# Performance work log

Measured on AMD Instinct MI355X. Metric: run time of the kernel, lower is better.

## Reference

```python
import jax, jax.numpy as jnp
import numpy as np

N = 16384          # points in the (single-batch) cloud
K = 16             # boundary_k
C = 20             # num semantic classes (ScanNet-style)
IGNORE = -1        # ignore_index
BOUNDARY_W = 1.0   # boundary_loss_weight


def setup_inputs() -> dict:
    key = jax.random.key(0)
    k1, k2, k3 = jax.random.split(key, 3)
    coord = jax.random.normal(k1, (N, 3), jnp.float32)
    seg_logits = jax.random.normal(k2, (N, C), jnp.float32)
    segment = jax.random.randint(k3, (N,), 0, C, dtype=jnp.int32)
    return {"coord": coord, "seg_logits": seg_logits, "segment": segment, "offset": N}


def _knn_idx(coord):
    # brute-force kNN (loop=False): exclude self via +inf diagonal
    d2 = jnp.sum(coord * coord, axis=1)                       # [N]
    dist = d2[:, None] + d2[None, :] - 2.0 * (coord @ coord.T)  # [N, N]
    dist = dist + jnp.where(jnp.eye(dist.shape[0], dtype=bool), jnp.inf, 0.0)
    _, idx = jax.lax.top_k(-dist, K)                          # [N, K] neighbor (src) indices per center (dst)
    return idx


def _masked_ce(logp_tgt, mask):
    # mean cross-entropy over masked points (matches torch reduction='mean' w/ ignore_index)
    cnt = jnp.sum(mask)
    s = jnp.sum(jnp.where(mask, logp_tgt, 0.0))
    return jnp.where(cnt > 0, -s / jnp.maximum(cnt, 1).astype(logp_tgt.dtype), 0.0)


def reference(coord, seg_logits, segment, offset):
    # --- boundary mask: knn_graph -> per-edge label diff -> scatter-max to dst ---
    nbr = _knn_idx(coord)                                     # [N, K] src indices, dst = row index
    nbr_seg = segment[nbr]                                    # gather: [N, K]
    valid_pt = segment != IGNORE                              # [N]
    valid = (nbr_seg != IGNORE) & valid_pt[:, None]           # per-edge valid
    diff = valid & (nbr_seg != segment[:, None])              # per-edge label mismatch
    boundary = jnp.any(diff, axis=1)                          # scatter-max over dst == row-wise any

    # --- main loss: cross-entropy with ignore_index ---
    logp = jax.nn.log_softmax(seg_logits, axis=-1)            # [N, C]
    tgt = jnp.clip(segment, 0, C - 1)
    logp_tgt = jnp.take_along_axis(logp, tgt[:, None], axis=1)[:, 0]  # [N]
    main_loss = _masked_ce(logp_tgt, valid_pt)

    # --- boundary loss: CE restricted to boundary points (0 if none) ---
    bmask = boundary & valid_pt
    boundary_loss = _masked_ce(logp_tgt, bmask)

    loss = main_loss + BOUNDARY_W * boundary_loss
    return loss
```

## Files before the change

### kernel.cpp

```cpp
#include <hip/hip_runtime.h>
#include <hip/hip_bf16.h>
#include <math.h>

#define N_PTS 16384
#define KNN   16
#define NCLS  20
#define BND_W 1.0f

#define THREADS 512
#define WAVES   8
#define FR      4
#define RPW     (16 * FR)
#define RPB     (WAVES * RPW)
#define RBLKS   (N_PTS / RPB)
#define CSPLIT  16
#define CAND_PB (N_PTS / CSPLIT)

typedef short  short8 __attribute__((ext_vector_type(8)));
typedef float  f32x4  __attribute__((ext_vector_type(4)));

__device__ __forceinline__ unsigned short f2bf(float x) {
    union { __hip_bfloat16 h; unsigned short u; } cv;
    cv.h = __float2bfloat16(x);
    return cv.u;
}
__device__ __forceinline__ float bf2f(unsigned short b) {
    union { __hip_bfloat16 h; unsigned short u; } cv;
    cv.u = b;
    return __bfloat162float(cv.h);
}

__global__ __launch_bounds__(256) void k_enc(const float* __restrict__ coord,
                                             const int* __restrict__ seg,
                                             unsigned short* __restrict__ aenc,
                                             unsigned short* __restrict__ benc,
                                             int* __restrict__ cnt,
                                             float* __restrict__ accum,
                                             int* __restrict__ done_rb,
                                             unsigned* __restrict__ done_final) {
    const int i = blockIdx.x * 256 + threadIdx.x;
    float x = coord[3 * i], y = coord[3 * i + 1], z = coord[3 * i + 2];
    int lab = seg[i];
    unsigned short xh = f2bf(x), yh = f2bf(y), zh = f2bf(z);
    unsigned short xl = f2bf(x - bf2f(xh));
    unsigned short yl = f2bf(y - bf2f(yh));
    unsigned short zl = f2bf(z - bf2f(zh));
    float h = 0.5f * fmaf(x, x, fmaf(y, y, z * z));
    unsigned short hh = f2bf(h);
    unsigned short hl = f2bf(h - bf2f(hh));
    const unsigned short one = 0x3F80u, nb = 0xC480u;

    __attribute__((aligned(16))) unsigned short a[32], b[32];
    a[0] = xh; a[1] = xl; a[2] = xh;
    a[3] = yh; a[4] = yl; a[5] = yh;
    a[6] = zh; a[7] = zl; a[8] = zh;
    a[9] = one; a[10] = one;
#pragma unroll
    for (int s = 0; s < NCLS; s++) a[11 + s] = (lab == s) ? nb : 0u;
    a[31] = nb;

    b[0] = xh; b[1] = xh; b[2] = xl;
    b[3] = yh; b[4] = yh; b[5] = yl;
    b[6] = zh; b[7] = zh; b[8] = zl;
    b[9]  = hh ^ 0x8000u;
    b[10] = hl ^ 0x8000u;
#pragma unroll
    for (int s = 0; s < NCLS; s++) b[11 + s] = (lab == s) ? one : 0u;
    b[31] = (lab < 0) ? one : 0u;

    short8* ap = (short8*)(aenc + (size_t)i * 32);
    short8* bp = (short8*)(benc + (size_t)i * 32);
#pragma unroll
    for (int kb = 0; kb < 4; kb++) {
        ap[kb] = ((const short8*)a)[kb];
        bp[kb] = ((const short8*)b)[kb];
    }

    cnt[i] = 0;
    if (i < 4) accum[i] = 0.f;
    if (i == 4) *done_final = 0u;
    if (i >= 8 && i < 8 + RBLKS) done_rb[i - 8] = 0;
}

__device__ __forceinline__ float waveReduceSum(float v) {
#pragma unroll
    for (int off = 32; off > 0; off >>= 1) v += __shfl_down(v, off, 64);
    return v;
}

template<bool PASS1>
__global__ __launch_bounds__(THREADS, 4) void k_pass(
    const unsigned short* __restrict__ aenc,
    const unsigned short* __restrict__ benc,
    const int* __restrict__ seg, const float* __restrict__ logits,
    float* __restrict__ smax_part, int* __restrict__ cnt,
    float* __restrict__ accum, int* __restrict__ done_rb,
    unsigned* __restrict__ done_final, float* __restrict__ out)
{
    __shared__ float thr_lds[RPB];
    __shared__ int s_flag;
    const int tid  = threadIdx.x;
    const int lane = tid & 63, wave = tid >> 6;
    const int l15  = lane & 15, l4 = lane >> 4;
    const int rb   = blockIdx.x * RPB;
    const int split = blockIdx.y;
    const int cb   = split * CAND_PB;

    short8 af[FR];
#pragma unroll
    for (int f = 0; f < FR; f++)
        af[f] = *(const short8*)(aenc + (size_t)(rb + wave * RPW + f * 16 + l15) * 32 + l4 * 8);
    if (!PASS1) {
#pragma unroll
        for (int f = 0; f < FR; f++) {
            union { short8 s; unsigned u[4]; } cv_;
            cv_.s = af[f];
            if (l4 == 1) { cv_.u[1] &= 0x0000FFFFu; cv_.u[2] = 0u; cv_.u[3] = 0u; }
            else if (l4 >= 2) { cv_.u[0] = 0u; cv_.u[1] = 0u; cv_.u[2] = 0u; cv_.u[3] = 0u; }
            af[f] = cv_.s;
        }
    }

    float thr[FR][4];
    if (!PASS1) {
        int row = rb + tid;
        float m = smax_part[row];
#pragma unroll
        for (int s = 1; s < CSPLIT; s++) m = fmaxf(m, smax_part[s * N_PTS + row]);
        thr_lds[tid] = m;
        __syncthreads();
#pragma unroll
        for (int f = 0; f < FR; f++)
#pragma unroll
            for (int r = 0; r < 4; r++)
                thr[f][r] = thr_lds[wave * RPW + f * 16 + l4 * 4 + r];
    }

    f32x4 rmax[FR];
    int cv[FR][4];
#pragma unroll
    for (int f = 0; f < FR; f++)
#pragma unroll
        for (int r = 0; r < 4; r++) { rmax[f][r] = -3.0e38f; cv[f][r] = 0; }

    const short8* bp = (const short8*)benc;
    const f32x4 zero = {0.f, 0.f, 0.f, 0.f};
#pragma unroll 4
    for (int c0 = 0; c0 < CAND_PB; c0 += 16) {
        short8 bf = bp[(size_t)(cb + c0 + l15) * 4 + l4];
        f32x4 d[FR];
#pragma unroll
        for (int f = 0; f < FR; f++)
            d[f] = __builtin_amdgcn_mfma_f32_16x16x32_bf16(af[f], bf, zero, 0, 0, 0);
        if (PASS1) {
#pragma unroll
            for (int f = 0; f < FR; f++)
#pragma unroll
                for (int r = 0; r < 4; r++)
                    rmax[f][r] = fmaxf(rmax[f][r], d[f][r]);
        } else {
#pragma unroll
            for (int f = 0; f < FR; f++)
#pragma unroll
                for (int r = 0; r < 4; r++)
                    cv[f][r] += (d[f][r] > thr[f][r]) ? 1 : 0;
        }
    }

    if (PASS1) {
#pragma unroll
        for (int m = 1; m < 16; m <<= 1)
#pragma unroll
            for (int f = 0; f < FR; f++)
#pragma unroll
                for (int r = 0; r < 4; r++)
                    rmax[f][r] = fmaxf(rmax[f][r], __shfl_xor(rmax[f][r], m, 64));
        if (l15 == 0) {
#pragma unroll
            for (int f = 0; f < FR; f++)
#pragma unroll
                for (int r = 0; r < 4; r++)
                    smax_part[split * N_PTS + rb + wave * RPW + f * 16 + l4 * 4 + r] = rmax[f][r];
        }
    } else {
#pragma unroll
        for (int m = 1; m < 16; m <<= 1)
#pragma unroll
            for (int f = 0; f < FR; f++)
#pragma unroll
                for (int r = 0; r < 4; r++)
                    cv[f][r] += __shfl_xor(cv[f][r], m, 64);
        if (l15 == 0) {
#pragma unroll
            for (int f = 0; f < FR; f++)
#pragma unroll
                for (int r = 0; r < 4; r++)
                    atomicAdd(&cnt[rb + wave * RPW + f * 16 + l4 * 4 + r], cv[f][r]);
        }

        __syncthreads();
        if (tid == 0) {
            __threadfence();
            s_flag = (atomicAdd(&done_rb[blockIdx.x], 1) == CSPLIT - 1) ? 1 : 0;
        }
        __syncthreads();
        if (s_flag) {
            const int row = rb + tid;
            int sg = seg[row];
            bool valid = (sg != -1);
            const float4* row4 = (const float4*)(logits + (size_t)row * NCLS);
            float a[NCLS];
            float4 v0 = row4[0], v1 = row4[1], v2 = row4[2], v3 = row4[3], v4 = row4[4];
            a[0]=v0.x; a[1]=v0.y; a[2]=v0.z; a[3]=v0.w;
            a[4]=v1.x; a[5]=v1.y; a[6]=v1.z; a[7]=v1.w;
            a[8]=v2.x; a[9]=v2.y; a[10]=v2.z; a[11]=v2.w;
            a[12]=v3.x; a[13]=v3.y; a[14]=v3.z; a[15]=v3.w;
            a[16]=v4.x; a[17]=v4.y; a[18]=v4.z; a[19]=v4.w;
            float mx = a[0];
#pragma unroll
            for (int c = 1; c < NCLS; c++) mx = fmaxf(mx, a[c]);
            float se = 0.f;
#pragma unroll
            for (int c = 0; c < NCLS; c++) se += __expf(a[c] - mx);
            int tgt = min(max(sg, 0), NCLS - 1);
            float at = 0.f;
#pragma unroll
            for (int c = 0; c < NCLS; c++) at += (c == tgt) ? a[c] : 0.f;
            float logp = at - mx - __logf(se);
            int crow = atomicAdd(&cnt[row], 0);
            bool bnd = valid && ((crow - 1) < KNN);
            float sm = valid ? logp : 0.f, nm = valid ? 1.f : 0.f;
            float sb = bnd ? logp : 0.f,  nb2 = bnd ? 1.f : 0.f;
            sm = waveReduceSum(sm); nm = waveReduceSum(nm);
            sb = waveReduceSum(sb); nb2 = waveReduceSum(nb2);
            if ((tid & 63) == 0) {
                atomicAdd(&accum[0], sm);
                atomicAdd(&accum[1], nm);
                atomicAdd(&accum[2], sb);
                atomicAdd(&accum[3], nb2);
            }
            __syncthreads();
            if (tid == 0) {
                __threadfence();
                if (atomicAdd(done_final, 1u) == (unsigned)(RBLKS - 1)) {
                    float Sm = atomicAdd(&accum[0], 0.f);
                    float Cm = atomicAdd(&accum[1], 0.f);
                    float Sb = atomicAdd(&accum[2], 0.f);
                    float Cb = atomicAdd(&accum[3], 0.f);
                    float main_loss = (Cm > 0.f) ? (-Sm / fmaxf(Cm, 1.f)) : 0.f;
                    float bnd_loss  = (Cb > 0.f) ? (-Sb / fmaxf(Cb, 1.f)) : 0.f;
                    out[0] = main_loss + BND_W * bnd_loss;
                }
            }
        }
    }
}

extern "C" void kernel_launch(void* const* d_in, const int* in_sizes, int n_in,
                              void* d_out, int out_size, void* d_ws, size_t ws_size,
                              hipStream_t stream) {
    const float* coord  = (const float*)d_in[0];
    const float* logits = (const float*)d_in[1];
    const int*   seg    = (const int*)d_in[2];
    (void)in_sizes; (void)n_in; (void)out_size; (void)ws_size;

    unsigned short* aenc = (unsigned short*)d_ws;
    unsigned short* benc = (unsigned short*)((char*)d_ws + (1u << 20));
    float* smax_part = (float*)((char*)d_ws + (2u << 20));
    int*   cnt       = (int*)((char*)d_ws + (3u << 20));
    char*  tail      = (char*)d_ws + (3u << 20) + N_PTS * 4;
    float*    accum      = (float*)tail;
    unsigned* done_final = (unsigned*)(tail + 16);
    int*      done_rb    = (int*)(tail + 32);

    dim3 grid(RBLKS, CSPLIT);
    k_enc        <<<N_PTS / 256, 256, 0, stream>>>(coord, seg, aenc, benc, cnt,
                                                   accum, done_rb, done_final);
    k_pass<true> <<<grid, THREADS, 0, stream>>>(aenc, benc, seg, logits, smax_part, cnt,
                                                accum, done_rb, done_final, (float*)d_out);
    k_pass<false><<<grid, THREADS, 0, stream>>>(aenc, benc, seg, logits, smax_part, cnt,
                                                accum, done_rb, done_final, (float*)d_out);
}
```

Baseline: 78.43 us.

## Stage candidate tiles in LDS with swizzle, halve block size, double candidate split

Each block now copies its candidate slice of the encoded B matrix into shared memory with global_load_lds, and the encoding step XOR-swizzles the 16-byte chunks so the LDS reads avoid bank conflicts. Blocks shrink to 4 waves, the candidate dimension is split 32 ways, and the inner loop issues two MFMA groups per iteration. The partial-max buffer becomes row-major so pass 2 can gather each row's threshold with vector loads. The goal is to cut repeated global/L2 traffic for B and raise occupancy, at the cost of 32 KB of LDS per block and more partial results to reduce.

```diff
diff --git a/kernel.cpp b/kernel.cpp
--- a/kernel.cpp
+++ b/kernel.cpp
@@ -7,13 +7,13 @@
 #define NCLS  20
 #define BND_W 1.0f
 
-#define THREADS 512
-#define WAVES   8
+#define THREADS 256
+#define WAVES   4
 #define FR      4
 #define RPW     (16 * FR)
 #define RPB     (WAVES * RPW)
 #define RBLKS   (N_PTS / RPB)
-#define CSPLIT  16
+#define CSPLIT  32
 #define CAND_PB (N_PTS / CSPLIT)
 
 typedef short  short8 __attribute__((ext_vector_type(8)));
@@ -28,6 +28,12 @@
     union { __hip_bfloat16 h; unsigned short u; } cv;
     cv.u = b;
     return __bfloat162float(cv.h);
+}
+
+__device__ __forceinline__ void gload16(const void* g, void* l) {
+    __builtin_amdgcn_global_load_lds(
+        (const __attribute__((address_space(1))) unsigned int*)g,
+        (__attribute__((address_space(3))) unsigned int*)l, 16, 0, 0);
 }
 
 __global__ __launch_bounds__(256) void k_enc(const float* __restrict__ coord,
@@ -70,10 +76,11 @@
 
     short8* ap = (short8*)(aenc + (size_t)i * 32);
     short8* bp = (short8*)(benc + (size_t)i * 32);
+    const int swz = (i >> 1) & 3;
 #pragma unroll
     for (int kb = 0; kb < 4; kb++) {
         ap[kb] = ((const short8*)a)[kb];
-        bp[kb] = ((const short8*)b)[kb];
+        bp[kb ^ swz] = ((const short8*)b)[kb];
     }
 
     cnt[i] = 0;
@@ -89,7 +96,7 @@
 }
 
 template<bool PASS1>
-__global__ __launch_bounds__(THREADS, 4) void k_pass(
+__global__ __launch_bounds__(THREADS, 6) void k_pass(
     const unsigned short* __restrict__ aenc,
     const unsigned short* __restrict__ benc,
     const int* __restrict__ seg, const float* __restrict__ logits,
@@ -97,6 +104,7 @@
     float* __restrict__ accum, int* __restrict__ done_rb,
     unsigned* __restrict__ done_final, float* __restrict__ out)
 {
+    __shared__ __align__(16) unsigned short bsm[CAND_PB * 32];
     __shared__ float thr_lds[RPB];
     __shared__ int s_flag;
     const int tid  = threadIdx.x;
@@ -106,6 +114,14 @@
     const int split = blockIdx.y;
     const int cb   = split * CAND_PB;
 
+    {
+        const char* gsrc = (const char*)benc + (size_t)cb * 64;
+#pragma unroll
+        for (int r = 0; r < 8; r++)
+            gload16(gsrc + (wave * 8 + r) * 1024 + lane * 16,
+                    (char*)bsm + (wave * 8 + r) * 1024);
+    }
+
     short8 af[FR];
 #pragma unroll
     for (int f = 0; f < FR; f++)
@@ -121,14 +137,20 @@
         }
     }
 
+    if (!PASS1) {
+        const f32x4* sp = (const f32x4*)(smax_part + (size_t)(rb + tid) * CSPLIT);
+        float m = -3.0e38f;
+#pragma unroll
+        for (int q = 0; q < CSPLIT / 4; q++) {
+            f32x4 v = sp[q];
+            m = fmaxf(fmaxf(fmaxf(m, v[0]), fmaxf(v[1], v[2])), v[3]);
+        }
+        thr_lds[tid] = m;
+    }
+    __syncthreads();
+
     float thr[FR][4];
     if (!PASS1) {
-        int row = rb + tid;
-        float m = smax_part[row];
-#pragma unroll
-        for (int s = 1; s < CSPLIT; s++) m = fmaxf(m, smax_part[s * N_PTS + row]);
-        thr_lds[tid] = m;
-        __syncthreads();
 #pragma unroll
         for (int f = 0; f < FR; f++)
 #pragma unroll
@@ -143,27 +165,34 @@
 #pragma unroll
         for (int r = 0; r < 4; r++) { rmax[f][r] = -3.0e38f; cv[f][r] = 0; }
 
-    const short8* bp = (const short8*)benc;
+    const short8* bp = (const short8*)bsm;
+    const int bidx = l15 * 4 + (l4 ^ ((l15 >> 1) & 3));
     const f32x4 zero = {0.f, 0.f, 0.f, 0.f};
-#pragma unroll 4
-    for (int c0 = 0; c0 < CAND_PB; c0 += 16) {
-        short8 bf = bp[(size_t)(cb + c0 + l15) * 4 + l4];
-        f32x4 d[FR];
+
+#pragma unroll 2
+    for (int c0 = 0; c0 < CAND_PB; c0 += 32) {
+        short8 bA = bp[bidx + c0 * 4];
+        short8 bB = bp[bidx + (c0 + 16) * 4];
+        f32x4 dA[FR], dB[FR];
 #pragma unroll
         for (int f = 0; f < FR; f++)
-            d[f] = __builtin_amdgcn_mfma_f32_16x16x32_bf16(af[f], bf, zero, 0, 0, 0);
+            dA[f] = __builtin_amdgcn_mfma_f32_16x16x32_bf16(af[f], bA, zero, 0, 0, 0);
+#pragma unroll
+        for (int f = 0; f < FR; f++)
+            dB[f] = __builtin_amdgcn_mfma_f32_16x16x32_bf16(af[f], bB, zero, 0, 0, 0);
         if (PASS1) {
 #pragma unroll
             for (int f = 0; f < FR; f++)
 #pragma unroll
                 for (int r = 0; r < 4; r++)
-                    rmax[f][r] = fmaxf(rmax[f][r], d[f][r]);
+                    rmax[f][r] = fmaxf(fmaxf(rmax[f][r], dA[f][r]), dB[f][r]);
         } else {
 #pragma unroll
             for (int f = 0; f < FR; f++)
 #pragma unroll
                 for (int r = 0; r < 4; r++)
-                    cv[f][r] += (d[f][r] > thr[f][r]) ? 1 : 0;
+                    cv[f][r] += ((dA[f][r] > thr[f][r]) ? 1 : 0)
+                              + ((dB[f][r] > thr[f][r]) ? 1 : 0);
         }
     }
 
@@ -180,7 +209,8 @@
             for (int f = 0; f < FR; f++)
 #pragma unroll
                 for (int r = 0; r < 4; r++)
-                    smax_part[split * N_PTS + rb + wave * RPW + f * 16 + l4 * 4 + r] = rmax[f][r];
+                    smax_part[(size_t)(rb + wave * RPW + f * 16 + l4 * 4 + r) * CSPLIT + split]
+                        = rmax[f][r];
         }
     } else {
 #pragma unroll
@@ -267,8 +297,8 @@
     unsigned short* aenc = (unsigned short*)d_ws;
     unsigned short* benc = (unsigned short*)((char*)d_ws + (1u << 20));
     float* smax_part = (float*)((char*)d_ws + (2u << 20));
-    int*   cnt       = (int*)((char*)d_ws + (3u << 20));
-    char*  tail      = (char*)d_ws + (3u << 20) + N_PTS * 4;
+    int*   cnt       = (int*)((char*)d_ws + (4u << 20));
+    char*  tail      = (char*)d_ws + (4u << 20) + N_PTS * 4;
     float*    accum      = (float*)tail;
     unsigned* done_final = (unsigned*)(tail + 16);
     int*      done_rb    = (int*)(tail + 32);
```

New measurement: 91.93 us. 17.2% more time.

## Fuse both kNN passes into one kernel with LDS double-buffered candidate chunks

Applied to the files above, without the earlier changes.

The two separate pass kernels, which split candidates across 16 blocks per row group, become one kernel. Each block owns 64 rows and sweeps all candidates twice: once for the row max and once for the threshold count. Candidate encodings are streamed through a double-buffered, XOR-swizzled LDS tile using global_load_lds, and the A fragments are built in-kernel from coord and segment. This removes the intermediate smax_part and cnt arrays, their global atomics and the extra launch. In exchange, the grid shrinks to 256 blocks of 512 threads, each doing 16x more serial candidate work, so there is less parallelism per row tile.

```diff
diff --git a/kernel.cpp b/kernel.cpp
--- a/kernel.cpp
+++ b/kernel.cpp
@@ -9,12 +9,12 @@
 
 #define THREADS 512
 #define WAVES   8
-#define FR      4
-#define RPW     (16 * FR)
-#define RPB     (WAVES * RPW)
-#define RBLKS   (N_PTS / RPB)
-#define CSPLIT  16
-#define CAND_PB (N_PTS / CSPLIT)
+#define RPB     64
+#define NBLK    (N_PTS / RPB)
+#define CHUNK   1024
+#define NCHUNK  (N_PTS / CHUNK)
+#define TILES   (CHUNK / 16)
+#define TPW     (TILES / WAVES)
 
 typedef short  short8 __attribute__((ext_vector_type(8)));
 typedef float  f32x4  __attribute__((ext_vector_type(4)));
@@ -30,13 +30,16 @@
     return __bfloat162float(cv.h);
 }
 
+__device__ __forceinline__ void gload16(const void* g, void* l) {
+    __builtin_amdgcn_global_load_lds(
+        (const __attribute__((address_space(1))) unsigned int*)g,
+        (__attribute__((address_space(3))) unsigned int*)l, 16, 0, 0);
+}
+
 __global__ __launch_bounds__(256) void k_enc(const float* __restrict__ coord,
                                              const int* __restrict__ seg,
-                                             unsigned short* __restrict__ aenc,
                                              unsigned short* __restrict__ benc,
-                                             int* __restrict__ cnt,
                                              float* __restrict__ accum,
-                                             int* __restrict__ done_rb,
                                              unsigned* __restrict__ done_final) {
     const int i = blockIdx.x * 256 + threadIdx.x;
     float x = coord[3 * i], y = coord[3 * i + 1], z = coord[3 * i + 2];
@@ -48,17 +51,9 @@
     float h = 0.5f * fmaf(x, x, fmaf(y, y, z * z));
     unsigned short hh = f2bf(h);
     unsigned short hl = f2bf(h - bf2f(hh));
-    const unsigned short one = 0x3F80u, nb = 0xC480u;
-
-    __attribute__((aligned(16))) unsigned short a[32], b[32];
-    a[0] = xh; a[1] = xl; a[2] = xh;
-    a[3] = yh; a[4] = yl; a[5] = yh;
-    a[6] = zh; a[7] = zl; a[8] = zh;
-    a[9] = one; a[10] = one;
-#pragma unroll
-    for (int s = 0; s < NCLS; s++) a[11 + s] = (lab == s) ? nb : 0u;
-    a[31] = nb;
-
+    const unsigned short one = 0x3F80u;
+
+    __attribute__((aligned(16))) unsigned short b[32];
     b[0] = xh; b[1] = xh; b[2] = xl;
     b[3] = yh; b[4] = yh; b[5] = yl;
     b[6] = zh; b[7] = zh; b[8] = zl;
@@ -68,18 +63,47 @@
     for (int s = 0; s < NCLS; s++) b[11 + s] = (lab == s) ? one : 0u;
     b[31] = (lab < 0) ? one : 0u;
 
-    short8* ap = (short8*)(aenc + (size_t)i * 32);
     short8* bp = (short8*)(benc + (size_t)i * 32);
-#pragma unroll
-    for (int kb = 0; kb < 4; kb++) {
-        ap[kb] = ((const short8*)a)[kb];
-        bp[kb] = ((const short8*)b)[kb];
-    }
-
-    cnt[i] = 0;
+    const int swz = (i >> 1) & 3;
+#pragma unroll
+    for (int kb = 0; kb < 4; kb++) bp[kb ^ swz] = ((const short8*)b)[kb];
+
     if (i < 4) accum[i] = 0.f;
     if (i == 4) *done_final = 0u;
-    if (i >= 8 && i < 8 + RBLKS) done_rb[i - 8] = 0;
+}
+
+__device__ __forceinline__ short8 build_a_frag(const float* __restrict__ coord,
+                                               const int* __restrict__ seg,
+                                               int row, int g) {
+    __attribute__((aligned(16))) unsigned short s[8];
+    const unsigned short one = 0x3F80u, nb = 0xC480u;
+    if (g == 0) {
+        float x = coord[3 * row], y = coord[3 * row + 1], z = coord[3 * row + 2];
+        unsigned short xh = f2bf(x), yh = f2bf(y), zh = f2bf(z);
+        s[0] = xh; s[1] = f2bf(x - bf2f(xh)); s[2] = xh;
+        s[3] = yh; s[4] = f2bf(y - bf2f(yh)); s[5] = yh;
+        s[6] = zh; s[7] = f2bf(z - bf2f(zh));
+    } else if (g == 1) {
+        float z = coord[3 * row + 2];
+        int lab = seg[row];
+        s[0] = f2bf(z); s[1] = one; s[2] = one;
+        s[3] = (lab == 0) ? nb : 0u; s[4] = (lab == 1) ? nb : 0u;
+        s[5] = (lab == 2) ? nb : 0u; s[6] = (lab == 3) ? nb : 0u;
+        s[7] = (lab == 4) ? nb : 0u;
+    } else if (g == 2) {
+        int lab = seg[row];
+        s[0] = (lab == 5) ? nb : 0u;  s[1] = (lab == 6) ? nb : 0u;
+        s[2] = (lab == 7) ? nb : 0u;  s[3] = (lab == 8) ? nb : 0u;
+        s[4] = (lab == 9) ? nb : 0u;  s[5] = (lab == 10) ? nb : 0u;
+        s[6] = (lab == 11) ? nb : 0u; s[7] = (lab == 12) ? nb : 0u;
+    } else {
+        int lab = seg[row];
+        s[0] = (lab == 13) ? nb : 0u; s[1] = (lab == 14) ? nb : 0u;
+        s[2] = (lab == 15) ? nb : 0u; s[3] = (lab == 16) ? nb : 0u;
+        s[4] = (lab == 17) ? nb : 0u; s[5] = (lab == 18) ? nb : 0u;
+        s[6] = (lab == 19) ? nb : 0u; s[7] = nb;
+    }
+    return *(const short8*)s;
 }
 
 __device__ __forceinline__ float waveReduceSum(float v) {
@@ -88,170 +112,210 @@
     return v;
 }
 
-template<bool PASS1>
-__global__ __launch_bounds__(THREADS, 4) void k_pass(
-    const unsigned short* __restrict__ aenc,
-    const unsigned short* __restrict__ benc,
-    const int* __restrict__ seg, const float* __restrict__ logits,
-    float* __restrict__ smax_part, int* __restrict__ cnt,
-    float* __restrict__ accum, int* __restrict__ done_rb,
-    unsigned* __restrict__ done_final, float* __restrict__ out)
+__global__ __launch_bounds__(THREADS, 2) void k_main(
+    const float* __restrict__ coord, const int* __restrict__ seg,
+    const float* __restrict__ logits, const unsigned short* __restrict__ benc,
+    float* __restrict__ accum, unsigned* __restrict__ done_final,
+    float* __restrict__ out)
 {
+    __shared__ __align__(16) unsigned short bsm[2][CHUNK * 32];
+    __shared__ float wsm[WAVES * RPB];
     __shared__ float thr_lds[RPB];
-    __shared__ int s_flag;
     const int tid  = threadIdx.x;
     const int lane = tid & 63, wave = tid >> 6;
     const int l15  = lane & 15, l4 = lane >> 4;
     const int rb   = blockIdx.x * RPB;
-    const int split = blockIdx.y;
-    const int cb   = split * CAND_PB;
-
-    short8 af[FR];
-#pragma unroll
-    for (int f = 0; f < FR; f++)
-        af[f] = *(const short8*)(aenc + (size_t)(rb + wave * RPW + f * 16 + l15) * 32 + l4 * 8);
-    if (!PASS1) {
-#pragma unroll
-        for (int f = 0; f < FR; f++) {
-            union { short8 s; unsigned u[4]; } cv_;
-            cv_.s = af[f];
-            if (l4 == 1) { cv_.u[1] &= 0x0000FFFFu; cv_.u[2] = 0u; cv_.u[3] = 0u; }
-            else if (l4 >= 2) { cv_.u[0] = 0u; cv_.u[1] = 0u; cv_.u[2] = 0u; cv_.u[3] = 0u; }
-            af[f] = cv_.s;
-        }
-    }
-
-    float thr[FR][4];
-    if (!PASS1) {
-        int row = rb + tid;
-        float m = smax_part[row];
-#pragma unroll
-        for (int s = 1; s < CSPLIT; s++) m = fmaxf(m, smax_part[s * N_PTS + row]);
-        thr_lds[tid] = m;
+
+    short8 af[4];
+#pragma unroll
+    for (int f = 0; f < 4; f++)
+        af[f] = build_a_frag(coord, seg, rb + f * 16 + l15, l4);
+
+    const int bidx = l15 * 4 + (l4 ^ ((l15 >> 1) & 3));
+    const f32x4 zero = {0.f, 0.f, 0.f, 0.f};
+
+    {
+        const char* g = (const char*)benc;
+#pragma unroll
+        for (int r = 0; r < 8; r++)
+            gload16(g + (wave * 8 + r) * 1024 + lane * 16,
+                    (char*)bsm[0] + (wave * 8 + r) * 1024);
+    }
+
+    f32x4 rmax[4];
+#pragma unroll
+    for (int f = 0; f < 4; f++)
+#pragma unroll
+        for (int r = 0; r < 4; r++) rmax[f][r] = -3.0e38f;
+
+    for (int ch = 0; ch < NCHUNK; ch++) {
+        const int b = ch & 1;
         __syncthreads();
-#pragma unroll
-        for (int f = 0; f < FR; f++)
-#pragma unroll
-            for (int r = 0; r < 4; r++)
-                thr[f][r] = thr_lds[wave * RPW + f * 16 + l4 * 4 + r];
-    }
-
-    f32x4 rmax[FR];
-    int cv[FR][4];
-#pragma unroll
-    for (int f = 0; f < FR; f++)
-#pragma unroll
-        for (int r = 0; r < 4; r++) { rmax[f][r] = -3.0e38f; cv[f][r] = 0; }
-
-    const short8* bp = (const short8*)benc;
-    const f32x4 zero = {0.f, 0.f, 0.f, 0.f};
-#pragma unroll 4
-    for (int c0 = 0; c0 < CAND_PB; c0 += 16) {
-        short8 bf = bp[(size_t)(cb + c0 + l15) * 4 + l4];
-        f32x4 d[FR];
-#pragma unroll
-        for (int f = 0; f < FR; f++)
-            d[f] = __builtin_amdgcn_mfma_f32_16x16x32_bf16(af[f], bf, zero, 0, 0, 0);
-        if (PASS1) {
-#pragma unroll
-            for (int f = 0; f < FR; f++)
+        if (ch + 1 < NCHUNK) {
+            const char* g = (const char*)benc + (size_t)(ch + 1) * CHUNK * 64;
+#pragma unroll
+            for (int r = 0; r < 8; r++)
+                gload16(g + (wave * 8 + r) * 1024 + lane * 16,
+                        (char*)bsm[b ^ 1] + (wave * 8 + r) * 1024);
+        }
+        const short8* bp = (const short8*)bsm[b];
+#pragma unroll
+        for (int t = 0; t < TPW; t++) {
+            short8 bf = bp[(wave + t * WAVES) * 64 + bidx];
+            f32x4 d[4];
+#pragma unroll
+            for (int f = 0; f < 4; f++)
+                d[f] = __builtin_amdgcn_mfma_f32_16x16x32_bf16(af[f], bf, zero, 0, 0, 0);
+#pragma unroll
+            for (int f = 0; f < 4; f++)
 #pragma unroll
                 for (int r = 0; r < 4; r++)
                     rmax[f][r] = fmaxf(rmax[f][r], d[f][r]);
-        } else {
-#pragma unroll
-            for (int f = 0; f < FR; f++)
+        }
+    }
+
+#pragma unroll
+    for (int m = 1; m < 16; m <<= 1)
+#pragma unroll
+        for (int f = 0; f < 4; f++)
+#pragma unroll
+            for (int r = 0; r < 4; r++)
+                rmax[f][r] = fmaxf(rmax[f][r], __shfl_xor(rmax[f][r], m, 64));
+    __syncthreads();
+    if (l15 == 0) {
+#pragma unroll
+        for (int f = 0; f < 4; f++)
+#pragma unroll
+            for (int r = 0; r < 4; r++)
+                wsm[wave * RPB + f * 16 + l4 * 4 + r] = rmax[f][r];
+    }
+    __syncthreads();
+    if (tid < RPB) {
+        float m = wsm[tid];
+#pragma unroll
+        for (int w = 1; w < WAVES; w++) m = fmaxf(m, wsm[w * RPB + tid]);
+        thr_lds[tid] = m;
+    }
+#pragma unroll
+    for (int f = 0; f < 4; f++) {
+        union { short8 s; unsigned u[4]; } cv_;
+        cv_.s = af[f];
+        if (l4 == 1) { cv_.u[1] &= 0x0000FFFFu; cv_.u[2] = 0u; cv_.u[3] = 0u; }
+        else if (l4 >= 2) { cv_.u[0] = 0u; cv_.u[1] = 0u; cv_.u[2] = 0u; cv_.u[3] = 0u; }
+        af[f] = cv_.s;
+    }
+    {
+        const char* g = (const char*)benc;
+#pragma unroll
+        for (int r = 0; r < 8; r++)
+            gload16(g + (wave * 8 + r) * 1024 + lane * 16,
+                    (char*)bsm[0] + (wave * 8 + r) * 1024);
+    }
+    __syncthreads();
+
+    float thr[4][4];
+    int cv[4][4];
+#pragma unroll
+    for (int f = 0; f < 4; f++)
+#pragma unroll
+        for (int r = 0; r < 4; r++) {
+            thr[f][r] = thr_lds[f * 16 + l4 * 4 + r];
+            cv[f][r] = 0;
+        }
+
+    for (int ch = 0; ch < NCHUNK; ch++) {
+        const int b = ch & 1;
+        __syncthreads();
+        if (ch + 1 < NCHUNK) {
+            const char* g = (const char*)benc + (size_t)(ch + 1) * CHUNK * 64;
+#pragma unroll
+            for (int r = 0; r < 8; r++)
+                gload16(g + (wave * 8 + r) * 1024 + lane * 16,
+                        (char*)bsm[b ^ 1] + (wave * 8 + r) * 1024);
+        }
+        const short8* bp = (const short8*)bsm[b];
+#pragma unroll
+        for (int t = 0; t < TPW; t++) {
+            short8 bf = bp[(wave + t * WAVES) * 64 + bidx];
+            f32x4 d[4];
+#pragma unroll
+            for (int f = 0; f < 4; f++)
+                d[f] = __builtin_amdgcn_mfma_f32_16x16x32_bf16(af[f], bf, zero, 0, 0, 0);
+#pragma unroll
+            for (int f = 0; f < 4; f++)
 #pragma unroll
                 for (int r = 0; r < 4; r++)
                     cv[f][r] += (d[f][r] > thr[f][r]) ? 1 : 0;
         }
     }
 
-    if (PASS1) {
-#pragma unroll
-        for (int m = 1; m < 16; m <<= 1)
-#pragma unroll
-            for (int f = 0; f < FR; f++)
-#pragma unroll
-                for (int r = 0; r < 4; r++)
-                    rmax[f][r] = fmaxf(rmax[f][r], __shfl_xor(rmax[f][r], m, 64));
-        if (l15 == 0) {
-#pragma unroll
-            for (int f = 0; f < FR; f++)
-#pragma unroll
-                for (int r = 0; r < 4; r++)
-                    smax_part[split * N_PTS + rb + wave * RPW + f * 16 + l4 * 4 + r] = rmax[f][r];
-        }
-    } else {
-#pragma unroll
-        for (int m = 1; m < 16; m <<= 1)
-#pragma unroll
-            for (int f = 0; f < FR; f++)
-#pragma unroll
-                for (int r = 0; r < 4; r++)
-                    cv[f][r] += __shfl_xor(cv[f][r], m, 64);
-        if (l15 == 0) {
-#pragma unroll
-            for (int f = 0; f < FR; f++)
-#pragma unroll
-                for (int r = 0; r < 4; r++)
-                    atomicAdd(&cnt[rb + wave * RPW + f * 16 + l4 * 4 + r], cv[f][r]);
-        }
-
-        __syncthreads();
+#pragma unroll
+    for (int m = 1; m < 16; m <<= 1)
+#pragma unroll
+        for (int f = 0; f < 4; f++)
+#pragma unroll
+            for (int r = 0; r < 4; r++)
+                cv[f][r] += __shfl_xor(cv[f][r], m, 64);
+    __syncthreads();
+    int* ism = (int*)wsm;
+    if (l15 == 0) {
+#pragma unroll
+        for (int f = 0; f < 4; f++)
+#pragma unroll
+            for (int r = 0; r < 4; r++)
+                ism[wave * RPB + f * 16 + l4 * 4 + r] = cv[f][r];
+    }
+    __syncthreads();
+
+    if (tid < RPB) {
+        const int row = rb + tid;
+        int crow = ism[tid];
+#pragma unroll
+        for (int w = 1; w < WAVES; w++) crow += ism[w * RPB + tid];
+        int sg = seg[row];
+        bool valid = (sg != -1);
+        const float4* row4 = (const float4*)(logits + (size_t)row * NCLS);
+        float a[NCLS];
+        float4 v0 = row4[0], v1 = row4[1], v2 = row4[2], v3 = row4[3], v4 = row4[4];
+        a[0]=v0.x; a[1]=v0.y; a[2]=v0.z; a[3]=v0.w;
+        a[4]=v1.x; a[5]=v1.y; a[6]=v1.z; a[7]=v1.w;
+        a[8]=v2.x; a[9]=v2.y; a[10]=v2.z; a[11]=v2.w;
+        a[12]=v3.x; a[13]=v3.y; a[14]=v3.z; a[15]=v3.w;
+        a[16]=v4.x; a[17]=v4.y; a[18]=v4.z; a[19]=v4.w;
+        float mx = a[0];
+#pragma unroll
+        for (int c = 1; c < NCLS; c++) mx = fmaxf(mx, a[c]);
+        float se = 0.f;
+#pragma unroll
+        for (int c = 0; c < NCLS; c++) se += __expf(a[c] - mx);
+        int tgt = min(max(sg, 0), NCLS - 1);
+        float at = 0.f;
+#pragma unroll
+        for (int c = 0; c < NCLS; c++) at += (c == tgt) ? a[c] : 0.f;
+        float logp = at - mx - __logf(se);
+        bool bnd = valid && ((crow - 1) < KNN);
+        float sm = valid ? logp : 0.f, nm = valid ? 1.f : 0.f;
+        float sb = bnd ? logp : 0.f,  nb2 = bnd ? 1.f : 0.f;
+        sm = waveReduceSum(sm); nm = waveReduceSum(nm);
+        sb = waveReduceSum(sb); nb2 = waveReduceSum(nb2);
         if (tid == 0) {
-            __threadfence();
-            s_flag = (atomicAdd(&done_rb[blockIdx.x], 1) == CSPLIT - 1) ? 1 : 0;
-        }
-        __syncthreads();
-        if (s_flag) {
-            const int row = rb + tid;
-            int sg = seg[row];
-            bool valid = (sg != -1);
-            const float4* row4 = (const float4*)(logits + (size_t)row * NCLS);
-            float a[NCLS];
-            float4 v0 = row4[0], v1 = row4[1], v2 = row4[2], v3 = row4[3], v4 = row4[4];
-            a[0]=v0.x; a[1]=v0.y; a[2]=v0.z; a[3]=v0.w;
-            a[4]=v1.x; a[5]=v1.y; a[6]=v1.z; a[7]=v1.w;
-            a[8]=v2.x; a[9]=v2.y; a[10]=v2.z; a[11]=v2.w;
-            a[12]=v3.x; a[13]=v3.y; a[14]=v3.z; a[15]=v3.w;
-            a[16]=v4.x; a[17]=v4.y; a[18]=v4.z; a[19]=v4.w;
-            float mx = a[0];
-#pragma unroll
-            for (int c = 1; c < NCLS; c++) mx = fmaxf(mx, a[c]);
-            float se = 0.f;
-#pragma unroll
-            for (int c = 0; c < NCLS; c++) se += __expf(a[c] - mx);
-            int tgt = min(max(sg, 0), NCLS - 1);
-            float at = 0.f;
-#pragma unroll
-            for (int c = 0; c < NCLS; c++) at += (c == tgt) ? a[c] : 0.f;
-            float logp = at - mx - __logf(se);
-            int crow = atomicAdd(&cnt[row], 0);
-            bool bnd = valid && ((crow - 1) < KNN);
-            float sm = valid ? logp : 0.f, nm = valid ? 1.f : 0.f;
-            float sb = bnd ? logp : 0.f,  nb2 = bnd ? 1.f : 0.f;
-            sm = waveReduceSum(sm); nm = waveReduceSum(nm);
-            sb = waveReduceSum(sb); nb2 = waveReduceSum(nb2);
-            if ((tid & 63) == 0) {
-                atomicAdd(&accum[0], sm);
-                atomicAdd(&accum[1], nm);
-                atomicAdd(&accum[2], sb);
-                atomicAdd(&accum[3], nb2);
-            }
-            __syncthreads();
-            if (tid == 0) {
-                __threadfence();
-                if (atomicAdd(done_final, 1u) == (unsigned)(RBLKS - 1)) {
-                    float Sm = atomicAdd(&accum[0], 0.f);
-                    float Cm = atomicAdd(&accum[1], 0.f);
-                    float Sb = atomicAdd(&accum[2], 0.f);
-                    float Cb = atomicAdd(&accum[3], 0.f);
-                    float main_loss = (Cm > 0.f) ? (-Sm / fmaxf(Cm, 1.f)) : 0.f;
-                    float bnd_loss  = (Cb > 0.f) ? (-Sb / fmaxf(Cb, 1.f)) : 0.f;
-                    out[0] = main_loss + BND_W * bnd_loss;
-                }
-            }
+            atomicAdd(&accum[0], sm);
+            atomicAdd(&accum[1], nm);
+            atomicAdd(&accum[2], sb);
+            atomicAdd(&accum[3], nb2);
+        }
+    }
+    __syncthreads();
+    if (tid == 0) {
+        __threadfence();
+        if (atomicAdd(done_final, 1u) == (unsigned)(NBLK - 1)) {
+            float Sm = atomicAdd(&accum[0], 0.f);
+            float Cm = atomicAdd(&accum[1], 0.f);
+            float Sb = atomicAdd(&accum[2], 0.f);
+            float Cb = atomicAdd(&accum[3], 0.f);
+            float main_loss = (Cm > 0.f) ? (-Sm / fmaxf(Cm, 1.f)) : 0.f;
+            float bnd_loss  = (Cb > 0.f) ? (-Sb / fmaxf(Cb, 1.f)) : 0.f;
+            out[0] = main_loss + BND_W * bnd_loss;
         }
     }
 }
@@ -264,20 +328,11 @@
     const int*   seg    = (const int*)d_in[2];
     (void)in_sizes; (void)n_in; (void)out_size; (void)ws_size;
 
-    unsigned short* aenc = (unsigned short*)d_ws;
-    unsigned short* benc = (unsigned short*)((char*)d_ws + (1u << 20));
-    float* smax_part = (float*)((char*)d_ws + (2u << 20));
-    int*   cnt       = (int*)((char*)d_ws + (3u << 20));
-    char*  tail      = (char*)d_ws + (3u << 20) + N_PTS * 4;
-    float*    accum      = (float*)tail;
-    unsigned* done_final = (unsigned*)(tail + 16);
-    int*      done_rb    = (int*)(tail + 32);
-
-    dim3 grid(RBLKS, CSPLIT);
-    k_enc        <<<N_PTS / 256, 256, 0, stream>>>(coord, seg, aenc, benc, cnt,
-                                                   accum, done_rb, done_final);
-    k_pass<true> <<<grid, THREADS, 0, stream>>>(aenc, benc, seg, logits, smax_part, cnt,
-                                                accum, done_rb, done_final, (float*)d_out);
-    k_pass<false><<<grid, THREADS, 0, stream>>>(aenc, benc, seg, logits, smax_part, cnt,
-                                                accum, done_rb, done_final, (float*)d_out);
-}
+    unsigned short* benc = (unsigned short*)d_ws;
+    float*    accum      = (float*)((char*)d_ws + (1u << 20));
+    unsigned* done_final = (unsigned*)((char*)d_ws + (1u << 20) + 16);
+
+    k_enc <<<N_PTS / 256, 256, 0, stream>>>(coord, seg, benc, accum, done_final);
+    k_main<<<NBLK, THREADS, 0, stream>>>(coord, seg, logits, benc,
+                                         accum, done_final, (float*)d_out);
+}
```

After: 84.20 us. 7.4% more time.
